# Optimization experiments

Measured on AMD Instinct MI355X. Metric: run time of the kernel, lower is better.

The kernel has to match this reference:

```python
import jax, jax.numpy as jnp
import numpy as np

# Static pyramid config (must match setup_inputs' source_shape / level_start)
LEVEL_SHAPES = [(100, 100), (50, 50), (25, 25), (13, 13)]
DIM = 256
N_HEAD = 8
HEAD_DIM = DIM // N_HEAD
N_LEVEL = 4
N_POINT = 4
DIM_FF = 1024
B = 8
Q = 2048
LEN_IN = sum(h * w for h, w in LEVEL_SHAPES)


def layer_norm(x, g, b, eps=1e-5):
    m = jnp.mean(x, axis=-1, keepdims=True)
    v = jnp.mean(jnp.square(x - m), axis=-1, keepdims=True)
    return (x - m) * jax.lax.rsqrt(v + eps) * g + b


def bilinear_sample(v_flat, loc, H, W):
    # v_flat: (BH, H*W, hd); loc: (BH, Q, P, 2) normalized [0,1] as (x, y)
    # grid_sample align_corners=False with zero padding: pixel = loc*size - 0.5
    x = loc[..., 0] * W - 0.5
    y = loc[..., 1] * H - 0.5
    x0 = jnp.floor(x)
    y0 = jnp.floor(y)
    wx = (x - x0)[..., None]
    wy = (y - y0)[..., None]
    x0i = x0.astype(jnp.int32)
    y0i = y0.astype(jnp.int32)

    def gather(xi, yi):
        valid = ((xi >= 0) & (xi < W) & (yi >= 0) & (yi < H)).astype(v_flat.dtype)
        idx = jnp.clip(yi, 0, H - 1) * W + jnp.clip(xi, 0, W - 1)  # (BH,Q,P)
        BH, Qq, P = idx.shape
        f = jnp.take_along_axis(v_flat, idx.reshape(BH, Qq * P, 1), axis=1)
        return f.reshape(BH, Qq, P, -1) * valid[..., None]

    g00 = gather(x0i, y0i)
    g01 = gather(x0i + 1, y0i)
    g10 = gather(x0i, y0i + 1)
    g11 = gather(x0i + 1, y0i + 1)
    top = g00 * (1.0 - wx) + g01 * wx
    bot = g10 * (1.0 - wx) + g11 * wx
    return top * (1.0 - wy) + bot * wy


def ms_deform_attn_core(value, loc, attn):
    # value: (B, Lin, nh, hd); loc: (B, Q, nh, L, P, 2); attn: (B, Q, nh, L, P)
    Bv, Lin, nh, hd = value.shape
    Qq = loc.shape[1]
    out = jnp.zeros((Bv * nh, Qq, hd), value.dtype)
    start = 0
    for l, (H, W) in enumerate(LEVEL_SHAPES):
        v = value[:, start:start + H * W]                       # (B, HW, nh, hd)
        v = v.transpose(0, 2, 1, 3).reshape(Bv * nh, H * W, hd)
        ll = loc[:, :, :, l].transpose(0, 2, 1, 3, 4).reshape(Bv * nh, Qq, N_POINT, 2)
        aa = attn[:, :, :, l].transpose(0, 2, 1, 3).reshape(Bv * nh, Qq, N_POINT, 1)
        samp = bilinear_sample(v, ll, H, W)                     # (B*nh, Q, P, hd)
        out = out + jnp.sum(samp * aa, axis=2)
        start += H * W
    return out.reshape(Bv, nh, Qq, hd).transpose(0, 2, 1, 3).reshape(Bv, Qq, nh * hd)


def setup_inputs() -> dict:
    key = jax.random.key(0)
    ks = jax.random.split(key, 24)
    std = 0.02
    inp = {
        'input': jax.random.normal(ks[0], (B, Q, DIM), jnp.float32),
        'pos': jax.random.normal(ks[1], (B, Q, DIM), jnp.float32),
        'reference_point': jax.random.uniform(ks[2], (B, Q, N_LEVEL, 2), jnp.float32),
        'source': jax.random.normal(ks[3], (B, LEN_IN, DIM), jnp.float32),
        'source_shape': jnp.array(LEVEL_SHAPES, jnp.int64),
        'level_start': jnp.array(np.cumsum([0] + [h * w for h, w in LEVEL_SHAPES[:-1]]), jnp.int64),
        'source_mask': jnp.zeros((B, LEN_IN), jnp.bool_),
        # LayerNorms
        'ln1_g': jnp.ones((DIM,), jnp.float32), 'ln1_b': jnp.zeros((DIM,), jnp.float32),
        'ln2_g': jnp.ones((DIM,), jnp.float32), 'ln2_b': jnp.zeros((DIM,), jnp.float32),
        # MSDeformAttn projections
        'Wv': std * jax.random.normal(ks[4], (DIM, DIM), jnp.float32), 'bv': jnp.zeros((DIM,), jnp.float32),
        'Woff': std * jax.random.normal(ks[5], (DIM, N_HEAD * N_LEVEL * N_POINT * 2), jnp.float32),
        'boff': 0.5 * jax.random.normal(ks[6], (N_HEAD * N_LEVEL * N_POINT * 2,), jnp.float32),
        'Wattn': std * jax.random.normal(ks[7], (DIM, N_HEAD * N_LEVEL * N_POINT), jnp.float32),
        'battn': jnp.zeros((N_HEAD * N_LEVEL * N_POINT,), jnp.float32),
        'Wout': std * jax.random.normal(ks[8], (DIM, DIM), jnp.float32), 'bout': jnp.zeros((DIM,), jnp.float32),
        # FFN
        'W1': std * jax.random.normal(ks[9], (DIM, DIM_FF), jnp.float32), 'b1': jnp.zeros((DIM_FF,), jnp.float32),
        'W2': std * jax.random.normal(ks[10], (DIM_FF, DIM), jnp.float32), 'b2': jnp.zeros((DIM,), jnp.float32),
    }
    return inp


def reference(input, pos, reference_point, source, source_shape, level_start, source_mask,
              ln1_g, ln1_b, ln2_g, ln2_b, Wv, bv, Woff, boff, Wattn, battn, Wout, bout,
              W1, b1, W2, b2):
    # ---- cross norm + pos ----
    q = layer_norm(input, ln1_g, ln1_b)
    qp = q + pos
    # ---- MSDeformAttn ----
    value = source @ Wv + bv
    value = jnp.where(source_mask[..., None], 0.0, value)
    value = value.reshape(B, LEN_IN, N_HEAD, HEAD_DIM)
    offsets = (qp @ Woff + boff).reshape(B, Q, N_HEAD, N_LEVEL, N_POINT, 2)
    attn = (qp @ Wattn + battn).reshape(B, Q, N_HEAD, N_LEVEL * N_POINT)
    attn = jax.nn.softmax(attn, axis=-1).reshape(B, Q, N_HEAD, N_LEVEL, N_POINT)
    # offset normalizer is (W, H) per level
    normalizer = jnp.array([[w, h] for h, w in LEVEL_SHAPES], jnp.float32)
    loc = reference_point[:, :, None, :, None, :] + offsets / normalizer[None, None, None, :, None, :]
    out = ms_deform_attn_core(value, loc, attn)
    out = out @ Wout + bout
    x = input + out  # dropout is identity in eval
    # ---- FFN ----
    h = layer_norm(x, ln2_g, ln2_b)
    h = jax.nn.relu(h @ W1 + b1) @ W2 + b2
    x = x + h
    return (x, loc)
```

## Files before the change

kernel.cpp:

```cpp
#include <hip/hip_runtime.h>
#include <hip/hip_bf16.h>
#include <cstdint>
#include <cstddef>

#define B_    8
#define Q_    2048
#define DIM_  256
#define NH    8
#define HD    32
#define NL    4
#define NP    4
#define DFF   1024
#define LEN_IN_ 13294
#define MV    (B_*LEN_IN_)
#define MVPAD 106368
#define MQ    (B_*Q_)

typedef unsigned short u16;
typedef unsigned int   u32;
typedef __attribute__((ext_vector_type(8))) short short8;
typedef __attribute__((ext_vector_type(4))) float f32x4v;
typedef __attribute__((ext_vector_type(4))) unsigned short u16x4;

static __device__ __forceinline__ u16 f2bf(float f){
  union { float f; unsigned u; } x; x.f = f;
  unsigned r = x.u + 0x7fffu + ((x.u >> 16) & 1u);
  return (u16)(r >> 16);
}

template<int EPI>
__global__ __launch_bounds__(256)
void gemm_k(const u16* __restrict__ A, const u16* __restrict__ Bt,
            const float* __restrict__ bias, const float* __restrict__ res,
            void* __restrict__ outp, int N, int K, int Mstore)
{
  __shared__ u16 As[128*64];
  __shared__ u16 Bs[128*64];
  const int t = threadIdx.x;
  const int l = t & 63, wid = t >> 6;
  const int wm = wid >> 1, wn = wid & 1;
  const int m0 = blockIdx.x * 128, n0 = blockIdx.y * 128;

  f32x4v acc[4][4];
#pragma unroll
  for (int i = 0; i < 4; ++i)
#pragma unroll
    for (int j = 0; j < 4; ++j) acc[i][j] = 0.f;

  const int nkt = K >> 6;
  for (int kt = 0; kt < nkt; ++kt) {
#pragma unroll
    for (int i = 0; i < 4; ++i) {
      int chunk = i * 256 + t;
      int row   = chunk >> 3;
      int c16   = chunk & 7;
      int sc    = c16 ^ (row & 7);
      const u16* ga = A  + (size_t)(m0 + row) * K + kt * 64 + sc * 8;
      __builtin_amdgcn_global_load_lds((const __attribute__((address_space(1))) void*)ga,
                                       (__attribute__((address_space(3))) void*)(As + chunk * 8), 16, 0, 0);
      const u16* gb = Bt + (size_t)(n0 + row) * K + kt * 64 + sc * 8;
      __builtin_amdgcn_global_load_lds((const __attribute__((address_space(1))) void*)gb,
                                       (__attribute__((address_space(3))) void*)(Bs + chunk * 8), 16, 0, 0);
    }
    __syncthreads();
#pragma unroll
    for (int kk = 0; kk < 2; ++kk) {
      short8 af[4], bfr[4];
      const int lr  = l & 15;
      const int c   = kk * 4 + (l >> 4);
      const int swz = c ^ (lr & 7);
#pragma unroll
      for (int mi = 0; mi < 4; ++mi) {
        int r = wm * 64 + mi * 16 + lr;
        af[mi] = *reinterpret_cast<const short8*>(As + (r * 8 + swz) * 8);
      }
#pragma unroll
      for (int ni = 0; ni < 4; ++ni) {
        int r = wn * 64 + ni * 16 + lr;
        bfr[ni] = *reinterpret_cast<const short8*>(Bs + (r * 8 + swz) * 8);
      }
#pragma unroll
      for (int mi = 0; mi < 4; ++mi)
#pragma unroll
        for (int ni = 0; ni < 4; ++ni)
          acc[mi][ni] = __builtin_amdgcn_mfma_f32_16x16x32_bf16(af[mi], bfr[ni], acc[mi][ni], 0, 0, 0);
    }
    __syncthreads();
  }

  const int lr4 = l >> 4;
#pragma unroll
  for (int mi = 0; mi < 4; ++mi) {
    int rowb = m0 + wm * 64 + mi * 16 + lr4 * 4;
#pragma unroll
    for (int ni = 0; ni < 4; ++ni) {
      int col = n0 + wn * 64 + ni * 16 + (l & 15);
      float bb = bias[col];
#pragma unroll
      for (int v = 0; v < 4; ++v) {
        int r = rowb + v;
        if (r < Mstore) {
          float cv = acc[mi][ni][v] + bb;
          if (EPI == 2) cv += res[(size_t)r * N + col];
          if (EPI == 3) cv = fmaxf(cv, 0.f);
          if (EPI == 0 || EPI == 2) ((float*)outp)[(size_t)r * N + col] = cv;
          else                      ((u16*)outp)[(size_t)r * N + col] = f2bf(cv);
        }
      }
    }
  }
}

__global__ void prep_weights(const float* __restrict__ Wv,   const float* __restrict__ Woff,
                             const float* __restrict__ Wattn,const float* __restrict__ Wout,
                             const float* __restrict__ W1,   const float* __restrict__ W2,
                             const float* __restrict__ boff, const float* __restrict__ battn,
                             u16* __restrict__ WvT, u16* __restrict__ WcombT,
                             u16* __restrict__ WoutT, u16* __restrict__ W1T,
                             u16* __restrict__ W2T, float* __restrict__ bcomb)
{
  const int gid = blockIdx.x * 256 + threadIdx.x;
  const int R0 = 65536, R1 = R0 + 98304, R2 = R1 + 65536, R3 = R2 + 262144,
            R4 = R3 + 262144, R5 = R4 + 384;
  if (gid < R0) {
    int n = gid >> 8, k = gid & 255;
    WvT[gid] = f2bf(Wv[(size_t)k * 256 + n]);
  } else if (gid < R1) {
    int lo = gid - R0, n = lo >> 8, k = lo & 255;
    float s = (n < 256) ? Woff[(size_t)k * 256 + n] : Wattn[(size_t)k * 128 + (n - 256)];
    WcombT[lo] = f2bf(s);
  } else if (gid < R2) {
    int lo = gid - R1, n = lo >> 8, k = lo & 255;
    WoutT[lo] = f2bf(Wout[(size_t)k * 256 + n]);
  } else if (gid < R3) {
    int lo = gid - R2, n = lo >> 8, k = lo & 255;
    W1T[lo] = f2bf(W1[(size_t)k * 1024 + n]);
  } else if (gid < R4) {
    int lo = gid - R3, n = lo >> 10, k = lo & 1023;
    W2T[lo] = f2bf(W2[(size_t)k * 256 + n]);
  } else if (gid < R5) {
    int lo = gid - R4;
    bcomb[lo] = (lo < 256) ? boff[lo] : battn[lo - 256];
  }
}

__global__ void cvt_src(const float* __restrict__ src, u16* __restrict__ dst)
{
  size_t gid = (size_t)blockIdx.x * 256 + threadIdx.x;
  size_t base = gid * 4;
  const size_t nsrc = (size_t)MV * DIM_;
  u16x4 o;
  if (base < nsrc) {
    const float4 v = reinterpret_cast<const float4*>(src)[gid];
    o.x = f2bf(v.x); o.y = f2bf(v.y); o.z = f2bf(v.z); o.w = f2bf(v.w);
  } else {
    o.x = 0; o.y = 0; o.z = 0; o.w = 0;
  }
  *reinterpret_cast<u16x4*>(dst + base) = o;
}

template<bool ADDPOS>
__global__ __launch_bounds__(256)
void ln_k(const float* __restrict__ x, const float* __restrict__ pos,
          const float* __restrict__ g, const float* __restrict__ b, u16* __restrict__ out)
{
  const int warp = threadIdx.x >> 6, l = threadIdx.x & 63;
  const int row = blockIdx.x * 4 + warp;
  const float4 xv = reinterpret_cast<const float4*>(x + (size_t)row * 256)[l];
  float s = xv.x + xv.y + xv.z + xv.w;
#pragma unroll
  for (int o = 32; o; o >>= 1) s += __shfl_xor(s, o);
  const float mean = s * (1.f / 256.f);
  const float d0 = xv.x - mean, d1 = xv.y - mean, d2 = xv.z - mean, d3 = xv.w - mean;
  float vs = d0 * d0 + d1 * d1 + d2 * d2 + d3 * d3;
#pragma unroll
  for (int o = 32; o; o >>= 1) vs += __shfl_xor(vs, o);
  const float rs = rsqrtf(vs * (1.f / 256.f) + 1e-5f);
  const float4 gv = reinterpret_cast<const float4*>(g)[l];
  const float4 bv = reinterpret_cast<const float4*>(b)[l];
  float o0 = d0 * rs * gv.x + bv.x;
  float o1 = d1 * rs * gv.y + bv.y;
  float o2 = d2 * rs * gv.z + bv.z;
  float o3 = d3 * rs * gv.w + bv.w;
  if (ADDPOS) {
    const float4 pv = reinterpret_cast<const float4*>(pos + (size_t)row * 256)[l];
    o0 += pv.x; o1 += pv.y; o2 += pv.z; o3 += pv.w;
  }
  u16x4 ov; ov.x = f2bf(o0); ov.y = f2bf(o1); ov.z = f2bf(o2); ov.w = f2bf(o3);
  reinterpret_cast<u16x4*>(out + (size_t)row * 256)[l] = ov;
}

__global__ __launch_bounds__(256)
void locsoft(const float* __restrict__ oa, const float* __restrict__ refpt,
             float* __restrict__ attnw, float* __restrict__ locout)
{
  const int gh = blockIdx.x * 256 + threadIdx.x;
  const int row = gh >> 3, h = gh & 7;
  const float* orow = oa + (size_t)row * 384;
  float v[16];
#pragma unroll
  for (int i = 0; i < 16; ++i) v[i] = orow[256 + h * 16 + i];
  float m = v[0];
#pragma unroll
  for (int i = 1; i < 16; ++i) m = fmaxf(m, v[i]);
  float s = 0.f;
#pragma unroll
  for (int i = 0; i < 16; ++i) { v[i] = __expf(v[i] - m); s += v[i]; }
  const float inv = 1.f / s;
  float* ap = attnw + (size_t)gh * 16;
#pragma unroll
  for (int i = 0; i < 16; ++i) ap[i] = v[i] * inv;
  float* lp = locout + (size_t)gh * 32;
#pragma unroll
  for (int i = 0; i < 16; ++i) {
    const int lv = i >> 2;
    const float rn = (lv == 0) ? (1.f / 100.f) : (lv == 1) ? (1.f / 50.f)
                   : (lv == 2) ? (1.f / 25.f) : (1.f / 13.f);
    const float ox = orow[h * 32 + i * 2 + 0];
    const float oy = orow[h * 32 + i * 2 + 1];
    const float rx = refpt[(size_t)row * 8 + lv * 2 + 0];
    const float ry = refpt[(size_t)row * 8 + lv * 2 + 1];
    lp[i * 2 + 0] = rx + ox * rn;
    lp[i * 2 + 1] = ry + oy * rn;
  }
}

__global__ __launch_bounds__(256)
void msdeform_k(const u16* __restrict__ value, const float* __restrict__ attnw,
                const float* __restrict__ loc, u16* __restrict__ outp)
{
  const int t = threadIdx.x;
  const int rloc = t >> 7;
  const int rem = t & 127;
  const int h = rem >> 4, p = rem & 15;
  const int row = blockIdx.x * 2 + rloc;
  const int b = row >> 11;
  const int lv = p >> 2;

  const float2 lxy = *reinterpret_cast<const float2*>(loc + (((size_t)row * 8 + h) * 16 + p) * 2);
  const float aw = attnw[((size_t)row * 8 + h) * 16 + p];
  const int Wl = (lv == 0) ? 100 : (lv == 1) ? 50 : (lv == 2) ? 25 : 13;
  const int st = (lv == 0) ? 0 : (lv == 1) ? 10000 : (lv == 2) ? 12500 : 13125;
  const float Wf = (float)Wl;
  const float xx = lxy.x * Wf - 0.5f, yy = lxy.y * Wf - 0.5f;
  const float xf = floorf(xx), yf = floorf(yy);
  const float wx = xx - xf, wy = yy - yf;
  const int x0 = (int)xf, y0 = (int)yf;
  const int xc0 = min(max(x0, 0), Wl - 1), xc1 = min(max(x0 + 1, 0), Wl - 1);
  const int yc0 = min(max(y0, 0), Wl - 1), yc1 = min(max(y0 + 1, 0), Wl - 1);
  const float vx0 = (x0 >= 0 && x0 < Wl) ? 1.f : 0.f;
  const float vx1 = (x0 + 1 >= 0 && x0 + 1 < Wl) ? 1.f : 0.f;
  const float vy0 = (y0 >= 0 && y0 < Wl) ? 1.f : 0.f;
  const float vy1 = (y0 + 1 >= 0 && y0 + 1 < Wl) ? 1.f : 0.f;
  const int o00 = st + yc0 * Wl + xc0, o01 = st + yc0 * Wl + xc1;
  const int o10 = st + yc1 * Wl + xc0, o11 = st + yc1 * Wl + xc1;
  const float w00 = aw * (1.f - wx) * (1.f - wy) * vx0 * vy0;
  const float w01 = aw * wx * (1.f - wy) * vx1 * vy0;
  const float w10 = aw * (1.f - wx) * wy * vx0 * vy1;
  const float w11 = aw * wx * wy * vx1 * vy1;

  const char* vbase = (const char*)value + (size_t)b * LEN_IN_ * 512 + (size_t)(h * 32 + p * 2) * 2;
  float a0 = 0.f, a1 = 0.f;
#pragma unroll
  for (int q = 0; q < 16; ++q) {
    const int   c00 = __shfl(o00, q, 16), c01 = __shfl(o01, q, 16);
    const int   c10 = __shfl(o10, q, 16), c11 = __shfl(o11, q, 16);
    const float u00 = __shfl(w00, q, 16), u01 = __shfl(w01, q, 16);
    const float u10 = __shfl(w10, q, 16), u11 = __shfl(w11, q, 16);
    const u32 g00 = *reinterpret_cast<const u32*>(vbase + (size_t)c00 * 512);
    const u32 g01 = *reinterpret_cast<const u32*>(vbase + (size_t)c01 * 512);
    const u32 g10 = *reinterpret_cast<const u32*>(vbase + (size_t)c10 * 512);
    const u32 g11 = *reinterpret_cast<const u32*>(vbase + (size_t)c11 * 512);
    union { u32 u; float f; } lo, hi;
    lo.u = g00 << 16; hi.u = g00 & 0xffff0000u; a0 += u00 * lo.f; a1 += u00 * hi.f;
    lo.u = g01 << 16; hi.u = g01 & 0xffff0000u; a0 += u01 * lo.f; a1 += u01 * hi.f;
    lo.u = g10 << 16; hi.u = g10 & 0xffff0000u; a0 += u10 * lo.f; a1 += u10 * hi.f;
    lo.u = g11 << 16; hi.u = g11 & 0xffff0000u; a0 += u11 * lo.f; a1 += u11 * hi.f;
  }
  const u32 res = ((u32)f2bf(a1) << 16) | (u32)f2bf(a0);
  reinterpret_cast<u32*>(outp)[(size_t)row * 128 + h * 16 + p] = res;
}

extern "C" void kernel_launch(void* const* d_in, const int* in_sizes, int n_in,
                              void* d_out, int out_size, void* d_ws, size_t ws_size,
                              hipStream_t stream)
{
  (void)in_sizes; (void)n_in; (void)out_size; (void)ws_size;
  const float* input  = (const float*)d_in[0];
  const float* pos    = (const float*)d_in[1];
  const float* refpt  = (const float*)d_in[2];
  const float* source = (const float*)d_in[3];
  const float* ln1_g  = (const float*)d_in[7];
  const float* ln1_b  = (const float*)d_in[8];
  const float* ln2_g  = (const float*)d_in[9];
  const float* ln2_b  = (const float*)d_in[10];
  const float* Wv     = (const float*)d_in[11];
  const float* bv     = (const float*)d_in[12];
  const float* Woff   = (const float*)d_in[13];
  const float* boff   = (const float*)d_in[14];
  const float* Wattn  = (const float*)d_in[15];
  const float* battn  = (const float*)d_in[16];
  const float* Wout   = (const float*)d_in[17];
  const float* bout   = (const float*)d_in[18];
  const float* W1     = (const float*)d_in[19];
  const float* b1     = (const float*)d_in[20];
  const float* W2     = (const float*)d_in[21];
  const float* b2     = (const float*)d_in[22];

  char* ws = (char*)d_ws;
  u16*   WvT    = (u16*)  (ws + 0);
  u16*   WcombT = (u16*)  (ws + 131072);
  u16*   WoutT  = (u16*)  (ws + 327680);
  u16*   W1T    = (u16*)  (ws + 458752);
  u16*   W2T    = (u16*)  (ws + 983040);
  float* bcomb  = (float*)(ws + 1507328);
  u16*   valueB = (u16*)  (ws + 1508864);
  u16*   hB     = (u16*)  (ws + 1508864);
  u16*   qpB    = (u16*)  (ws + 55969280);
  u16*   msout  = (u16*)  (ws + 55969280);
  float* attnw  = (float*)(ws + 64357888);
  float* xbuf   = (float*)(ws + 72746496);
  u16*   xnB    = (u16*)  (ws + 89523712);
  u16*   srcB   = (u16*)  (ws + 97912320);
  float* oa     = (float*)(ws + 97912320);

  float* out_x   = (float*)d_out;
  float* out_loc = (float*)d_out + (size_t)MQ * DIM_;

  hipLaunchKernelGGL(prep_weights, dim3(2946), dim3(256), 0, stream,
                     Wv, Woff, Wattn, Wout, W1, W2, boff, battn,
                     WvT, WcombT, WoutT, W1T, W2T, bcomb);

  hipLaunchKernelGGL(cvt_src, dim3((MVPAD * DIM_) / 1024), dim3(256), 0, stream, source, srcB);

  hipLaunchKernelGGL((ln_k<true>), dim3(MQ / 4), dim3(256), 0, stream, input, pos, ln1_g, ln1_b, qpB);

  hipLaunchKernelGGL((gemm_k<1>), dim3(MVPAD / 128, 2), dim3(256), 0, stream,
                     srcB, WvT, bv, (const float*)nullptr, (void*)valueB, 256, 256, MV);

  hipLaunchKernelGGL((gemm_k<0>), dim3(MQ / 128, 3), dim3(256), 0, stream,
                     qpB, WcombT, bcomb, (const float*)nullptr, (void*)oa, 384, 256, MQ);

  hipLaunchKernelGGL(locsoft, dim3(MQ * NH / 256), dim3(256), 0, stream, oa, refpt, attnw, out_loc);

  hipLaunchKernelGGL(msdeform_k, dim3(MQ / 2), dim3(256), 0, stream, valueB, attnw, out_loc, msout);

  hipLaunchKernelGGL((gemm_k<2>), dim3(MQ / 128, 2), dim3(256), 0, stream,
                     msout, WoutT, bout, input, (void*)xbuf, 256, 256, MQ);

  hipLaunchKernelGGL((ln_k<false>), dim3(MQ / 4), dim3(256), 0, stream, xbuf, (const float*)nullptr, ln2_g, ln2_b, xnB);

  hipLaunchKernelGGL((gemm_k<3>), dim3(MQ / 128, DFF / 128), dim3(256), 0, stream,
                     xnB, W1T, b1, (const float*)nullptr, (void*)hB, DFF, 256, MQ);

  hipLaunchKernelGGL((gemm_k<2>), dim3(MQ / 128, 2), dim3(256), 0, stream,
                     hB, W2T, b2, xbuf, (void*)out_x, 256, 1024, MQ);
}
```

Measured before the change: 459.9 us.

## Fuse source bf16 conversion into value GEMM and softmax/loc into sampler

Drops the separate cvt_src pass by letting the value-projection GEMM load fp32 source rows directly and convert them to bf16 in registers before writing to LDS. It also removes the locsoft kernel by computing the per-head softmax with 16-lane shuffles and the sampling locations inside msdeform_k. This avoids a full write and read of a bf16 copy of source, plus the attention-weight buffer and one extra kernel launch. In exchange the value GEMM loses its async global_load_lds path for A and does its conversion on the GEMM's critical path.

```diff
diff --git a/kernel.cpp b/kernel.cpp
--- a/kernel.cpp
+++ b/kernel.cpp
@@ -28,9 +28,9 @@
   return (u16)(r >> 16);
 }
 
-template<int EPI>
+template<int EPI, bool AF32>
 __global__ __launch_bounds__(256)
-void gemm_k(const u16* __restrict__ A, const u16* __restrict__ Bt,
+void gemm_k(const void* __restrict__ Ap, const u16* __restrict__ Bt,
             const float* __restrict__ bias, const float* __restrict__ res,
             void* __restrict__ outp, int N, int K, int Mstore)
 {
@@ -55,9 +55,23 @@
       int row   = chunk >> 3;
       int c16   = chunk & 7;
       int sc    = c16 ^ (row & 7);
-      const u16* ga = A  + (size_t)(m0 + row) * K + kt * 64 + sc * 8;
-      __builtin_amdgcn_global_load_lds((const __attribute__((address_space(1))) void*)ga,
-                                       (__attribute__((address_space(3))) void*)(As + chunk * 8), 16, 0, 0);
+      if (AF32) {
+        const int gr = m0 + row;
+        float4 f0 = {0.f,0.f,0.f,0.f}, f1 = {0.f,0.f,0.f,0.f};
+        if (gr < Mstore) {
+          const float* ga = (const float*)Ap + (size_t)gr * K + kt * 64 + sc * 8;
+          f0 = *reinterpret_cast<const float4*>(ga);
+          f1 = *reinterpret_cast<const float4*>(ga + 4);
+        }
+        short8 pk;
+        pk[0]=(short)f2bf(f0.x); pk[1]=(short)f2bf(f0.y); pk[2]=(short)f2bf(f0.z); pk[3]=(short)f2bf(f0.w);
+        pk[4]=(short)f2bf(f1.x); pk[5]=(short)f2bf(f1.y); pk[6]=(short)f2bf(f1.z); pk[7]=(short)f2bf(f1.w);
+        *reinterpret_cast<short8*>(As + chunk * 8) = pk;
+      } else {
+        const u16* ga = (const u16*)Ap + (size_t)(m0 + row) * K + kt * 64 + sc * 8;
+        __builtin_amdgcn_global_load_lds((const __attribute__((address_space(1))) void*)ga,
+                                         (__attribute__((address_space(3))) void*)(As + chunk * 8), 16, 0, 0);
+      }
       const u16* gb = Bt + (size_t)(n0 + row) * K + kt * 64 + sc * 8;
       __builtin_amdgcn_global_load_lds((const __attribute__((address_space(1))) void*)gb,
                                        (__attribute__((address_space(3))) void*)(Bs + chunk * 8), 16, 0, 0);
@@ -144,21 +158,6 @@
   }
 }
 
-__global__ void cvt_src(const float* __restrict__ src, u16* __restrict__ dst)
-{
-  size_t gid = (size_t)blockIdx.x * 256 + threadIdx.x;
-  size_t base = gid * 4;
-  const size_t nsrc = (size_t)MV * DIM_;
-  u16x4 o;
-  if (base < nsrc) {
-    const float4 v = reinterpret_cast<const float4*>(src)[gid];
-    o.x = f2bf(v.x); o.y = f2bf(v.y); o.z = f2bf(v.z); o.w = f2bf(v.w);
-  } else {
-    o.x = 0; o.y = 0; o.z = 0; o.w = 0;
-  }
-  *reinterpret_cast<u16x4*>(dst + base) = o;
-}
-
 template<bool ADDPOS>
 __global__ __launch_bounds__(256)
 void ln_k(const float* __restrict__ x, const float* __restrict__ pos,
@@ -191,43 +190,9 @@
 }
 
 __global__ __launch_bounds__(256)
-void locsoft(const float* __restrict__ oa, const float* __restrict__ refpt,
-             float* __restrict__ attnw, float* __restrict__ locout)
-{
-  const int gh = blockIdx.x * 256 + threadIdx.x;
-  const int row = gh >> 3, h = gh & 7;
-  const float* orow = oa + (size_t)row * 384;
-  float v[16];
-#pragma unroll
-  for (int i = 0; i < 16; ++i) v[i] = orow[256 + h * 16 + i];
-  float m = v[0];
-#pragma unroll
-  for (int i = 1; i < 16; ++i) m = fmaxf(m, v[i]);
-  float s = 0.f;
-#pragma unroll
-  for (int i = 0; i < 16; ++i) { v[i] = __expf(v[i] - m); s += v[i]; }
-  const float inv = 1.f / s;
-  float* ap = attnw + (size_t)gh * 16;
-#pragma unroll
-  for (int i = 0; i < 16; ++i) ap[i] = v[i] * inv;
-  float* lp = locout + (size_t)gh * 32;
-#pragma unroll
-  for (int i = 0; i < 16; ++i) {
-    const int lv = i >> 2;
-    const float rn = (lv == 0) ? (1.f / 100.f) : (lv == 1) ? (1.f / 50.f)
-                   : (lv == 2) ? (1.f / 25.f) : (1.f / 13.f);
-    const float ox = orow[h * 32 + i * 2 + 0];
-    const float oy = orow[h * 32 + i * 2 + 1];
-    const float rx = refpt[(size_t)row * 8 + lv * 2 + 0];
-    const float ry = refpt[(size_t)row * 8 + lv * 2 + 1];
-    lp[i * 2 + 0] = rx + ox * rn;
-    lp[i * 2 + 1] = ry + oy * rn;
-  }
-}
-
-__global__ __launch_bounds__(256)
-void msdeform_k(const u16* __restrict__ value, const float* __restrict__ attnw,
-                const float* __restrict__ loc, u16* __restrict__ outp)
+void msdeform_k(const u16* __restrict__ value, const float* __restrict__ oa,
+                const float* __restrict__ refpt, float* __restrict__ locout,
+                u16* __restrict__ outp)
 {
   const int t = threadIdx.x;
   const int rloc = t >> 7;
@@ -236,13 +201,32 @@
   const int row = blockIdx.x * 2 + rloc;
   const int b = row >> 11;
   const int lv = p >> 2;
-
-  const float2 lxy = *reinterpret_cast<const float2*>(loc + (((size_t)row * 8 + h) * 16 + p) * 2);
-  const float aw = attnw[((size_t)row * 8 + h) * 16 + p];
+  const float* orow = oa + (size_t)row * 384;
+
+  const float araw = orow[256 + h * 16 + p];
+  float mx = araw;
+#pragma unroll
+  for (int o = 1; o < 16; o <<= 1) mx = fmaxf(mx, __shfl_xor(mx, o, 16));
+  const float e = __expf(araw - mx);
+  float se = e;
+#pragma unroll
+  for (int o = 1; o < 16; o <<= 1) se += __shfl_xor(se, o, 16);
+  const float aw = e / se;
+
+  const float2 off = *reinterpret_cast<const float2*>(orow + h * 32 + p * 2);
+  const float rn = (lv == 0) ? (1.f / 100.f) : (lv == 1) ? (1.f / 50.f)
+                 : (lv == 2) ? (1.f / 25.f) : (1.f / 13.f);
+  const float rx = refpt[(size_t)row * 8 + lv * 2 + 0];
+  const float ry = refpt[(size_t)row * 8 + lv * 2 + 1];
+  const float lx = rx + off.x * rn;
+  const float ly = ry + off.y * rn;
+  float2 lw; lw.x = lx; lw.y = ly;
+  *reinterpret_cast<float2*>(locout + (((size_t)row * 8 + h) * 16 + p) * 2) = lw;
+
   const int Wl = (lv == 0) ? 100 : (lv == 1) ? 50 : (lv == 2) ? 25 : 13;
   const int st = (lv == 0) ? 0 : (lv == 1) ? 10000 : (lv == 2) ? 12500 : 13125;
   const float Wf = (float)Wl;
-  const float xx = lxy.x * Wf - 0.5f, yy = lxy.y * Wf - 0.5f;
+  const float xx = lx * Wf - 0.5f, yy = ly * Wf - 0.5f;
   const float xf = floorf(xx), yf = floorf(yy);
   const float wx = xx - xf, wy = yy - yf;
   const int x0 = (int)xf, y0 = (int)yf;
@@ -318,11 +302,9 @@
   u16*   hB     = (u16*)  (ws + 1508864);
   u16*   qpB    = (u16*)  (ws + 55969280);
   u16*   msout  = (u16*)  (ws + 55969280);
-  float* attnw  = (float*)(ws + 64357888);
-  float* xbuf   = (float*)(ws + 72746496);
-  u16*   xnB    = (u16*)  (ws + 89523712);
-  u16*   srcB   = (u16*)  (ws + 97912320);
-  float* oa     = (float*)(ws + 97912320);
+  float* oa     = (float*)(ws + 64357888);
+  float* xbuf   = (float*)(ws + 89523712);
+  u16*   xnB    = (u16*)  (ws + 106300928);
 
   float* out_x   = (float*)d_out;
   float* out_loc = (float*)d_out + (size_t)MQ * DIM_;
@@ -331,28 +313,25 @@
                      Wv, Woff, Wattn, Wout, W1, W2, boff, battn,
                      WvT, WcombT, WoutT, W1T, W2T, bcomb);
 
-  hipLaunchKernelGGL(cvt_src, dim3((MVPAD * DIM_) / 1024), dim3(256), 0, stream, source, srcB);
-
   hipLaunchKernelGGL((ln_k<true>), dim3(MQ / 4), dim3(256), 0, stream, input, pos, ln1_g, ln1_b, qpB);
 
-  hipLaunchKernelGGL((gemm_k<1>), dim3(MVPAD / 128, 2), dim3(256), 0, stream,
-                     srcB, WvT, bv, (const float*)nullptr, (void*)valueB, 256, 256, MV);
-
-  hipLaunchKernelGGL((gemm_k<0>), dim3(MQ / 128, 3), dim3(256), 0, stream,
-                     qpB, WcombT, bcomb, (const float*)nullptr, (void*)oa, 384, 256, MQ);
-
-  hipLaunchKernelGGL(locsoft, dim3(MQ * NH / 256), dim3(256), 0, stream, oa, refpt, attnw, out_loc);
-
-  hipLaunchKernelGGL(msdeform_k, dim3(MQ / 2), dim3(256), 0, stream, valueB, attnw, out_loc, msout);
-
-  hipLaunchKernelGGL((gemm_k<2>), dim3(MQ / 128, 2), dim3(256), 0, stream,
-                     msout, WoutT, bout, input, (void*)xbuf, 256, 256, MQ);
+  hipLaunchKernelGGL((gemm_k<1, true>), dim3(MVPAD / 128, 2), dim3(256), 0, stream,
+                     (const void*)source, WvT, bv, (const float*)nullptr, (void*)valueB, 256, 256, MV);
+
+  hipLaunchKernelGGL((gemm_k<0, false>), dim3(MQ / 128, 3), dim3(256), 0, stream,
+                     (const void*)qpB, WcombT, bcomb, (const float*)nullptr, (void*)oa, 384, 256, MQ);
+
+  hipLaunchKernelGGL(msdeform_k, dim3(MQ / 2), dim3(256), 0, stream,
+                     valueB, oa, refpt, out_loc, msout);
+
+  hipLaunchKernelGGL((gemm_k<2, false>), dim3(MQ / 128, 2), dim3(256), 0, stream,
+                     (const void*)msout, WoutT, bout, input, (void*)xbuf, 256, 256, MQ);
 
   hipLaunchKernelGGL((ln_k<false>), dim3(MQ / 4), dim3(256), 0, stream, xbuf, (const float*)nullptr, ln2_g, ln2_b, xnB);
 
-  hipLaunchKernelGGL((gemm_k<3>), dim3(MQ / 128, DFF / 128), dim3(256), 0, stream,
-                     xnB, W1T, b1, (const float*)nullptr, (void*)hB, DFF, 256, MQ);
-
-  hipLaunchKernelGGL((gemm_k<2>), dim3(MQ / 128, 2), dim3(256), 0, stream,
-                     hB, W2T, b2, xbuf, (void*)out_x, 256, 1024, MQ);
-}
+  hipLaunchKernelGGL((gemm_k<3, false>), dim3(MQ / 128, DFF / 128), dim3(256), 0, stream,
+                     (const void*)xnB, W1T, b1, (const float*)nullptr, (void*)hB, DFF, 256, MQ);
+
+  hipLaunchKernelGGL((gemm_k<2, false>), dim3(MQ / 128, 2), dim3(256), 0, stream,
+                     (const void*)hB, W2T, b2, xbuf, (void*)out_x, 256, 1024, MQ);
+}
```

New measurement: 430.6 us. 1.07x faster.
